# Kernel tuning notes

Hardware: AMD Instinct MI355X
Metric: run time of the kernel (lower is better)

## Reference

```python
import jax, jax.numpy as jnp
import numpy as np

B, N, E, FIN, H, D = 256, 1024, 8192, 8, 4, 5
HD = H * D            # GATv2: 4 heads * 5 dim, concat -> 20
OBS = N               # flattened obs length
AOUT = 64             # action_space_output_dim (aggregator output)
HID = 256             # hidden_size
NOUT = 64             # num_outputs (logits)
NEG = 0.2             # GATv2 leaky_relu negative slope
EPS = 1e-5            # batchnorm eps


def setup_inputs() -> dict:
    key = jax.random.key(0)
    ks = jax.random.split(key, 16)
    def lin(k, i, o):
        return (jax.random.normal(k, (i, o), jnp.float32) / np.sqrt(i)).astype(jnp.float32)
    return {
        "x": jax.random.normal(ks[0], (B, N, FIN), jnp.float32),
        "obs": jax.random.normal(ks[1], (B, OBS), jnp.float32),
        "edge_index": jax.random.randint(ks[2], (2, E), 0, N),
        # GATv2 layer 0 (in=FIN) and layer 1 (in=HD)
        "Wl0": lin(ks[3], FIN, HD), "Wr0": lin(ks[4], FIN, HD),
        "att0": (jax.random.normal(ks[5], (H, D), jnp.float32) * 0.1), "b0": jnp.zeros((HD,), jnp.float32),
        "Wl1": lin(ks[6], HD, HD), "Wr1": lin(ks[7], HD, HD),
        "att1": (jax.random.normal(ks[8], (H, D), jnp.float32) * 0.1), "b1": jnp.zeros((HD,), jnp.float32),
        # BatchNorm params per layer (over feature dim)
        "g0": jnp.ones((HD,), jnp.float32), "be0": jnp.zeros((HD,), jnp.float32),
        "g1": jnp.ones((HD,), jnp.float32), "be1": jnp.zeros((HD,), jnp.float32),
        # aggregator linear (mean pool -> action-space dim)
        "Wagg": lin(ks[9], HD, AOUT), "bagg": jnp.zeros((AOUT,), jnp.float32),
        # logits MLP: cat(agg, obs) -> HID -> HID//2 -> NOUT (tanh activations)
        "W1": lin(ks[10], AOUT + OBS, HID), "bh1": jnp.zeros((HID,), jnp.float32),
        "W2": lin(ks[11], HID, HID // 2), "bh2": jnp.zeros((HID // 2,), jnp.float32),
        "Wout": lin(ks[12], HID // 2, NOUT), "bout": jnp.zeros((NOUT,), jnp.float32),
    }


def _gatv2_single(x, src, dst, Wl, Wr, att, bias):
    # x: [N, Fin]; src/dst: [Es] (with self loops)
    xl = (x @ Wl).reshape(N, H, D)
    xr = (x @ Wr).reshape(N, H, D)
    m = jax.nn.leaky_relu(xl[src] + xr[dst], NEG)        # [Es, H, D]
    e = jnp.einsum('ehd,hd->eh', m, att)                 # [Es, H]
    emax = jax.ops.segment_max(e, dst, num_segments=N)   # every node has a self loop
    p = jnp.exp(e - emax[dst])
    s = jax.ops.segment_sum(p, dst, num_segments=N)
    alpha = p / s[dst]                                   # softmax over incoming edges
    out = jax.ops.segment_sum(alpha[:, :, None] * xl[src], dst, num_segments=N)
    return out.reshape(N, HD) + bias


def _bn(x, g, b):
    # training-mode batchnorm over all (batch, node) positions, per feature
    mu = x.mean(axis=(0, 1))
    var = x.var(axis=(0, 1))
    return (x - mu) * jax.lax.rsqrt(var + EPS) * g + b


def reference(x, obs, edge_index, Wl0, Wr0, att0, b0, Wl1, Wr1, att1, b1,
              g0, be0, g1, be1, Wagg, bagg, W1, bh1, W2, bh2, Wout, bout):
    loops = jnp.arange(N)
    src = jnp.concatenate([edge_index[0], loops])
    dst = jnp.concatenate([edge_index[1], loops])
    layer = lambda xb, Wl, Wr, att, bias: jax.vmap(
        lambda xn: _gatv2_single(xn, src, dst, Wl, Wr, att, bias))(xb)
    h = layer(x, Wl0, Wr0, att0, b0)       # [B, N, HD]
    h = _bn(h, g0, be0)
    h = layer(h, Wl1, Wr1, att1, b1)
    h = _bn(h, g1, be1)
    agg = h.mean(axis=1) @ Wagg + bagg     # mean graph pooling -> [B, AOUT]
    f = jnp.concatenate([agg, obs], axis=1)
    f = jnp.tanh(f @ W1 + bh1)
    f = jnp.tanh(f @ W2 + bh2)
    return f @ Wout + bout                 # logits [B, NOUT]
```

## Files before the change

### kernel.cpp

```cpp
#include <hip/hip_runtime.h>
#include <hip/hip_bf16.h>
#include <math.h>

typedef unsigned short u16;
typedef __attribute__((ext_vector_type(8))) short short8;
typedef __attribute__((ext_vector_type(4))) float floatx4;

constexpr int kN   = 1024;
constexpr int kB   = 256;
constexpr int kE   = 8192;
constexpr int kHD  = 20;
constexpr float kEps = 1e-5f;

static __device__ __forceinline__ float u16_bf16_to_f32(u16 v) {
  return __uint_as_float(((unsigned)v) << 16);
}
static __device__ __forceinline__ void unpack2(unsigned u, float& a, float& b) {
  a = __uint_as_float(u << 16);
  b = __uint_as_float(u & 0xffff0000u);
}
static __device__ __forceinline__ u16 f2bf(float f) {
  __hip_bfloat16 h = __float2bfloat16(f);
  return *reinterpret_cast<u16*>(&h);
}
static __device__ __forceinline__ unsigned pack_bf16(float a, float b) {
  return (unsigned)f2bf(a) | ((unsigned)f2bf(b) << 16);
}

static __device__ __forceinline__ int detect_flag(const unsigned* __restrict__ x) {
  __shared__ int sflag;
  int t = threadIdx.x;
  if (t < 64) {
    unsigned w = x[t];
    unsigned e = (w >> 7) & 0xFFu;
    unsigned long long bl = __ballot(e >= 114u && e <= 136u);
    if (t == 0) sflag = (__popcll(bl) >= 32) ? 1 : 0;
  }
  __syncthreads();
  return sflag;
}

struct SmallConv {
  const void* src[17];
  float* dst[17];
  int n[17];
};

struct PrepArgs {
  const unsigned* x;
  const int* ei;
  const void* W1; const void* W2; const void* Wout;
  SmallConv sc;
  float* x_f;
  u16* W1p; u16* W2p; u16* Woutp;
  int* csr_off; int* csr_src;
  float* sums;
};

static __device__ __forceinline__ void repack_one(const void* src, u16* dst, int c, int N, int srcbf) {
  int n = c % N;
  int t2 = c / N;
  int q = t2 & 3, kb = t2 >> 2;
  int k0 = kb * 32 + q * 8;
  u16 w[8];
  if (srcbf) {
    const u16* s = (const u16*)src;
#pragma unroll
    for (int j = 0; j < 8; j++) w[j] = s[(size_t)(k0 + j) * N + n];
  } else {
    const float* s = (const float*)src;
#pragma unroll
    for (int j = 0; j < 8; j++) w[j] = f2bf(s[(size_t)(k0 + j) * N + n]);
  }
  uint4 out;
  out.x = (unsigned)w[0] | ((unsigned)w[1] << 16);
  out.y = (unsigned)w[2] | ((unsigned)w[3] << 16);
  out.z = (unsigned)w[4] | ((unsigned)w[5] << 16);
  out.w = (unsigned)w[6] | ((unsigned)w[7] << 16);
  *((uint4*)(dst + (size_t)c * 8)) = out;
}

__global__ __launch_bounds__(256) void prep_kernel(PrepArgs pa) {
  int bid = blockIdx.x;
  int t = threadIdx.x;
  if (bid == 0) {
    __shared__ int cnt[kN];
    __shared__ int cur[kN];
    __shared__ int wsum[4];
    for (int i = t; i < kN; i += 256) cnt[i] = 0;
    __syncthreads();
    for (int e = t; e < kE; e += 256) atomicAdd(&cnt[pa.ei[kE + e]], 1);
    __syncthreads();
    int d[4], pre[4];
    int s = 0;
#pragma unroll
    for (int j = 0; j < 4; j++) { d[j] = cnt[t * 4 + j] + 1; pre[j] = s; s += d[j]; }
    int lane = t & 63;
    int v = s;
    for (int o = 1; o < 64; o <<= 1) { int u = __shfl_up(v, o); if (lane >= o) v += u; }
    if (lane == 63) wsum[t >> 6] = v;
    __syncthreads();
    int wbase = 0;
    for (int w = 0; w < (t >> 6); w++) wbase += wsum[w];
    int base = wbase + v - s;
#pragma unroll
    for (int j = 0; j < 4; j++) {
      pa.csr_off[t * 4 + j] = base + pre[j];
      cur[t * 4 + j] = base + pre[j];
    }
    if (t == 255) pa.csr_off[kN] = wbase + v;
    __syncthreads();
    for (int e = t; e < kE; e += 256) {
      int sv = pa.ei[e], dv = pa.ei[kE + e];
      int pos = atomicAdd(&cur[dv], 1);
      pa.csr_src[pos] = sv;
    }
    for (int i = t; i < kN; i += 256) {
      int pos = atomicAdd(&cur[i], 1);
      pa.csr_src[pos] = i;
    }
    return;
  }
  int flag = detect_flag(pa.x);
  if (bid == 1) {
    for (int i = t; i < 640; i += 256) pa.sums[i] = 0.f;
    for (int k = 0; k < 17; k++) {
      int n = pa.sc.n[k];
      float* d = pa.sc.dst[k];
      if (flag) {
        const u16* s = (const u16*)pa.sc.src[k];
        for (int i = t; i < n; i += 256) d[i] = u16_bf16_to_f32(s[i]);
      } else {
        const float* s = (const float*)pa.sc.src[k];
        for (int i = t; i < n; i += 256) d[i] = s[i];
      }
    }
    return;
  }
  if (bid < 158) {
    int c = (bid - 2) * 256 + t;
    if (c < 34816) repack_one(pa.W1, pa.W1p, c, 256, flag);
    else if (c < 34816 + 4096) repack_one(pa.W2, pa.W2p, c - 34816, 128, flag);
    else if (c < 34816 + 4096 + 1024) repack_one(pa.Wout, pa.Woutp, c - 34816 - 4096, 64, flag);
    return;
  }
  int rid = (bid - 158) * 256 + t;
  int b = rid >> 10, n = rid & 1023;
  float v[8];
  if (flag) {
    uint4 r = *((const uint4*)((const u16*)pa.x + (size_t)rid * 8));
    unpack2(r.x, v[0], v[1]); unpack2(r.y, v[2], v[3]);
    unpack2(r.z, v[4], v[5]); unpack2(r.w, v[6], v[7]);
  } else {
    const float4* s = (const float4*)((const float*)pa.x + (size_t)rid * 8);
    float4 r0 = s[0], r1 = s[1];
    v[0] = r0.x; v[1] = r0.y; v[2] = r0.z; v[3] = r0.w;
    v[4] = r1.x; v[5] = r1.y; v[6] = r1.z; v[7] = r1.w;
  }
  float* d = pa.x_f + ((size_t)n * kB + b) * 8;
  ((float4*)d)[0] = make_float4(v[0], v[1], v[2], v[3]);
  ((float4*)d)[1] = make_float4(v[4], v[5], v[6], v[7]);
}

__global__ __launch_bounds__(256) void lin0_kernel(const float* __restrict__ x_f,
                                                   const float* __restrict__ Wl,
                                                   u16* __restrict__ xlb) {
  __shared__ float wl[160];
  int t = threadIdx.x;
  if (t < 160) wl[t] = Wl[t];
  __syncthreads();
  int n = blockIdx.x, b = t;
  const float4* xp = (const float4*)(x_f + ((size_t)n * kB + b) * 8);
  float xi[8];
  {
    float4 v0 = xp[0], v1 = xp[1];
    xi[0] = v0.x; xi[1] = v0.y; xi[2] = v0.z; xi[3] = v0.w;
    xi[4] = v1.x; xi[5] = v1.y; xi[6] = v1.z; xi[7] = v1.w;
  }
  float ol[kHD];
#pragma unroll
  for (int f = 0; f < kHD; f++) {
    float al = 0.f;
#pragma unroll
    for (int i = 0; i < 8; i++) al = fmaf(xi[i], wl[i * kHD + f], al);
    ol[f] = al;
  }
  uint2* pl = (uint2*)(xlb + ((size_t)n * kB + b) * kHD);
#pragma unroll
  for (int k = 0; k < 5; k++)
    pl[k] = make_uint2(pack_bf16(ol[4 * k], ol[4 * k + 1]), pack_bf16(ol[4 * k + 2], ol[4 * k + 3]));
}

__global__ __launch_bounds__(256) void lin1_kernel(const u16* __restrict__ hb,
                                                   const float* __restrict__ sums0,
                                                   const float* __restrict__ g0,
                                                   const float* __restrict__ be0,
                                                   const float* __restrict__ Wl1,
                                                   u16* __restrict__ xlb) {
  __shared__ float wl[400], sbl[kHD], afold[kHD], cfold[kHD], tot[2 * kHD];
  int t = threadIdx.x;
  if (t < 2 * kHD) {
    float v = 0.f;
    for (int k = 0; k < 8; k++) v += sums0[k * 2 * kHD + t];
    tot[t] = v;
  }
  __syncthreads();
  if (t < kHD) {
    const float inv = 1.0f / (float)(kN * kB);
    float mu = tot[t] * inv;
    float var = tot[kHD + t] * inv - mu * mu;
    float a = g0[t] * rsqrtf(var + kEps);
    afold[t] = a;
    cfold[t] = be0[t] - mu * a;
  }
  __syncthreads();
  for (int idx = t; idx < 400; idx += 256) wl[idx] = afold[idx / kHD] * Wl1[idx];
  if (t < kHD) {
    float s = 0.f;
    for (int f = 0; f < kHD; f++) s += cfold[f] * Wl1[f * kHD + t];
    sbl[t] = s;
  }
  __syncthreads();
  int n = blockIdx.x, b = t;
  float hv[kHD];
  {
    const uint2* p = (const uint2*)(hb + ((size_t)n * kB + b) * kHD);
#pragma unroll
    for (int k = 0; k < 5; k++) {
      uint2 v = p[k];
      unpack2(v.x, hv[4 * k], hv[4 * k + 1]);
      unpack2(v.y, hv[4 * k + 2], hv[4 * k + 3]);
    }
  }
  float ol[kHD];
#pragma unroll
  for (int j = 0; j < kHD; j++) {
    float al = sbl[j];
#pragma unroll
    for (int f = 0; f < kHD; f++) al = fmaf(hv[f], wl[f * kHD + j], al);
    ol[j] = al;
  }
  uint2* pl = (uint2*)(xlb + ((size_t)n * kB + b) * kHD);
#pragma unroll
  for (int k = 0; k < 5; k++)
    pl[k] = make_uint2(pack_bf16(ol[4 * k], ol[4 * k + 1]), pack_bf16(ol[4 * k + 2], ol[4 * k + 3]));
}

static __device__ __forceinline__ void attn_core(const u16* __restrict__ xlb,
                                                 const int* __restrict__ csr_src,
                                                 const int* __restrict__ ssrc,
                                                 int beg, int deg, int b,
                                                 const float* satt, const float* sbias,
                                                 float (&red)[2][2 * kHD],
                                                 int n, int bsw,
                                                 u16* __restrict__ hout,
                                                 float* __restrict__ sums) {
  float xrv[kHD];
  (void)xrv;
}

__global__ __launch_bounds__(128) void attn0_kernel(const u16* __restrict__ xlb,
                                                    const float* __restrict__ x_f,
                                                    const float* __restrict__ Wr0,
                                                    const float* __restrict__ att,
                                                    const float* __restrict__ bias,
                                                    const int* __restrict__ csr_off,
                                                    const int* __restrict__ csr_src,
                                                    u16* __restrict__ hout,
                                                    float* __restrict__ sums) {
  __shared__ float satt[kHD], sbias[kHD], swr[160];
  __shared__ float red[2][2 * kHD];
  __shared__ int ssrc[128];
  int t = threadIdx.x;
  if (t < kHD) { satt[t] = att[t]; sbias[t] = bias[t]; }
  for (int i = t; i < 160; i += 128) swr[i] = Wr0[i];
  int n = blockIdx.x >> 1;
  int beg = csr_off[n], end = csr_off[n + 1];
  int deg = end - beg;
  for (int i = t; i < deg && i < 128; i += 128) ssrc[i] = csr_src[beg + i];
  __syncthreads();
  int b = ((blockIdx.x & 1) << 7) | t;
  float xrv[kHD];
  {
    const float4* xp = (const float4*)(x_f + ((size_t)n * kB + b) * 8);
    float4 v0 = xp[0], v1 = xp[1];
    float xi[8] = {v0.x, v0.y, v0.z, v0.w, v1.x, v1.y, v1.z, v1.w};
#pragma unroll
    for (int f = 0; f < kHD; f++) {
      float a = 0.f;
#pragma unroll
      for (int i = 0; i < 8; i++) a = fmaf(xi[i], swr[i * kHD + f], a);
      xrv[f] = a;
    }
  }
  float s[4] = {0.f, 0.f, 0.f, 0.f};
  float acc[kHD];
#pragma unroll
  for (int f = 0; f < kHD; f++) acc[f] = 0.f;

  auto loadrow = [&](int i, uint2 (&rr)[5]) {
    int srcn = (i < 128) ? ssrc[i] : csr_src[beg + i];
    const uint2* p = (const uint2*)(xlb + ((size_t)srcn * kB + b) * kHD);
#pragma unroll
    for (int k = 0; k < 5; k++) rr[k] = p[k];
  };
  auto consume = [&](uint2 (&rr)[5]) {
    float xs[kHD];
#pragma unroll
    for (int k = 0; k < 5; k++) {
      unpack2(rr[k].x, xs[4 * k], xs[4 * k + 1]);
      unpack2(rr[k].y, xs[4 * k + 2], xs[4 * k + 3]);
    }
#pragma unroll
    for (int hh = 0; hh < 4; hh++) {
      float e = 0.f;
#pragma unroll
      for (int d2 = 0; d2 < 5; d2++) {
        int f = hh * 5 + d2;
        float v = xs[f] + xrv[f];
        v = fmaxf(v, 0.2f * v);
        e = fmaf(v, satt[f], e);
      }
      float p = __expf(e);
      s[hh] += p;
#pragma unroll
      for (int d2 = 0; d2 < 5; d2++) {
        int f = hh * 5 + d2;
        acc[f] = fmaf(p, xs[f], acc[f]);
      }
    }
  };

  uint2 r0[5], r1[5];
  loadrow(0, r0);
  if (deg > 1) loadrow(1, r1);
  int i = 0;
  for (; i + 1 < deg; i += 2) {
    consume(r0);
    if (i + 2 < deg) loadrow(i + 2, r0);
    consume(r1);
    if (i + 3 < deg) loadrow(i + 3, r1);
  }
  if (i < deg) consume(r0);

  float hv[kHD];
#pragma unroll
  for (int hh = 0; hh < 4; hh++) {
    float inv = 1.f / s[hh];
#pragma unroll
    for (int d2 = 0; d2 < 5; d2++) {
      int f = hh * 5 + d2;
      hv[f] = fmaf(acc[f], inv, sbias[f]);
    }
  }
  {
    uint2* ph = (uint2*)(hout + ((size_t)n * kB + b) * kHD);
#pragma unroll
    for (int k = 0; k < 5; k++)
      ph[k] = make_uint2(pack_bf16(hv[4 * k], hv[4 * k + 1]), pack_bf16(hv[4 * k + 2], hv[4 * k + 3]));
  }
  int lane = t & 63, wv = t >> 6;
#pragma unroll
  for (int f = 0; f < kHD; f++) {
    float a = hv[f], q = hv[f] * hv[f];
    for (int o = 32; o > 0; o >>= 1) { a += __shfl_down(a, o); q += __shfl_down(q, o); }
    if (lane == 0) { red[wv][f] = a; red[wv][kHD + f] = q; }
  }
  __syncthreads();
  if (t < 2 * kHD) atomicAdd(&sums[(blockIdx.x & 7) * 2 * kHD + t], red[0][t] + red[1][t]);
}

__global__ __launch_bounds__(128) void attn1_kernel(const u16* __restrict__ xlb,
                                                    const u16* __restrict__ hb,
                                                    const float* __restrict__ sums0,
                                                    const float* __restrict__ g0,
                                                    const float* __restrict__ be0,
                                                    const float* __restrict__ Wr1,
                                                    const float* __restrict__ att,
                                                    const float* __restrict__ bias,
                                                    const int* __restrict__ csr_off,
                                                    const int* __restrict__ csr_src,
                                                    u16* __restrict__ hout,
                                                    float* __restrict__ sums) {
  __shared__ float satt[kHD], sbias[kHD], swr[400], sbr[kHD];
  __shared__ float afold[kHD], cfold[kHD], tot[2 * kHD];
  __shared__ float red[2][2 * kHD];
  __shared__ int ssrc[128];
  int t = threadIdx.x;
  if (t < kHD) { satt[t] = att[t]; sbias[t] = bias[t]; }
  if (t >= 64 && t < 64 + 2 * kHD) {
    int j = t - 64;
    float v = 0.f;
    for (int k = 0; k < 8; k++) v += sums0[k * 2 * kHD + j];
    tot[j] = v;
  }
  int n = blockIdx.x >> 1;
  int beg = csr_off[n], end = csr_off[n + 1];
  int deg = end - beg;
  for (int i = t; i < deg && i < 128; i += 128) ssrc[i] = csr_src[beg + i];
  __syncthreads();
  if (t < kHD) {
    const float inv = 1.0f / (float)(kN * kB);
    float mu = tot[t] * inv;
    float var = tot[kHD + t] * inv - mu * mu;
    float a = g0[t] * rsqrtf(var + kEps);
    afold[t] = a;
    cfold[t] = be0[t] - mu * a;
  }
  __syncthreads();
  for (int idx = t; idx < 400; idx += 128) swr[idx] = afold[idx / kHD] * Wr1[idx];
  if (t < kHD) {
    float sv = 0.f;
    for (int f = 0; f < kHD; f++) sv = fmaf(cfold[f], Wr1[f * kHD + t], sv);
    sbr[t] = sv;
  }
  __syncthreads();
  int b = ((blockIdx.x & 1) << 7) | t;
  float xrv[kHD];
  {
    float hv0[kHD];
    const uint2* p = (const uint2*)(hb + ((size_t)n * kB + b) * kHD);
#pragma unroll
    for (int k = 0; k < 5; k++) {
      uint2 v = p[k];
      unpack2(v.x, hv0[4 * k], hv0[4 * k + 1]);
      unpack2(v.y, hv0[4 * k + 2], hv0[4 * k + 3]);
    }
#pragma unroll
    for (int j = 0; j < kHD; j++) {
      float a = sbr[j];
#pragma unroll
      for (int f = 0; f < kHD; f++) a = fmaf(hv0[f], swr[f * kHD + j], a);
      xrv[j] = a;
    }
  }
  float s[4] = {0.f, 0.f, 0.f, 0.f};
  float acc[kHD];
#pragma unroll
  for (int f = 0; f < kHD; f++) acc[f] = 0.f;

  auto loadrow = [&](int i, uint2 (&rr)[5]) {
    int srcn = (i < 128) ? ssrc[i] : csr_src[beg + i];
    const uint2* p = (const uint2*)(xlb + ((size_t)srcn * kB + b) * kHD);
#pragma unroll
    for (int k = 0; k < 5; k++) rr[k] = p[k];
  };
  auto consume = [&](uint2 (&rr)[5]) {
    float xs[kHD];
#pragma unroll
    for (int k = 0; k < 5; k++) {
      unpack2(rr[k].x, xs[4 * k], xs[4 * k + 1]);
      unpack2(rr[k].y, xs[4 * k + 2], xs[4 * k + 3]);
    }
#pragma unroll
    for (int hh = 0; hh < 4; hh++) {
      float e = 0.f;
#pragma unroll
      for (int d2 = 0; d2 < 5; d2++) {
        int f = hh * 5 + d2;
        float v = xs[f] + xrv[f];
        v = fmaxf(v, 0.2f * v);
        e = fmaf(v, satt[f], e);
      }
      float p = __expf(e);
      s[hh] += p;
#pragma unroll
      for (int d2 = 0; d2 < 5; d2++) {
        int f = hh * 5 + d2;
        acc[f] = fmaf(p, xs[f], acc[f]);
      }
    }
  };

  uint2 r0[5], r1[5];
  loadrow(0, r0);
  if (deg > 1) loadrow(1, r1);
  int i = 0;
  for (; i + 1 < deg; i += 2) {
    consume(r0);
    if (i + 2 < deg) loadrow(i + 2, r0);
    consume(r1);
    if (i + 3 < deg) loadrow(i + 3, r1);
  }
  if (i < deg) consume(r0);

  float hv[kHD];
#pragma unroll
  for (int hh = 0; hh < 4; hh++) {
    float inv = 1.f / s[hh];
#pragma unroll
    for (int d2 = 0; d2 < 5; d2++) {
      int f = hh * 5 + d2;
      hv[f] = fmaf(acc[f], inv, sbias[f]);
    }
  }
  {
    uint2* ph = (uint2*)(hout + ((size_t)n * kB + b) * kHD);
#pragma unroll
    for (int k = 0; k < 5; k++)
      ph[k] = make_uint2(pack_bf16(hv[4 * k], hv[4 * k + 1]), pack_bf16(hv[4 * k + 2], hv[4 * k + 3]));
  }
  int lane = t & 63, wv = t >> 6;
#pragma unroll
  for (int f = 0; f < kHD; f++) {
    float a = hv[f], q = hv[f] * hv[f];
    for (int o = 32; o > 0; o >>= 1) { a += __shfl_down(a, o); q += __shfl_down(q, o); }
    if (lane == 0) { red[wv][f] = a; red[wv][kHD + f] = q; }
  }
  __syncthreads();
  if (t < 2 * kHD) atomicAdd(&sums[(blockIdx.x & 7) * 2 * kHD + t], red[0][t] + red[1][t]);
}

__global__ __launch_bounds__(256) void pool_fin_kernel(const u16* __restrict__ hb,
                                                       const float* __restrict__ sums,
                                                       const float* __restrict__ g1,
                                                       const float* __restrict__ be1,
                                                       const float* __restrict__ Wagg,
                                                       const float* __restrict__ bagg,
                                                       const void* __restrict__ obsraw,
                                                       const unsigned* __restrict__ xdet,
                                                       u16* __restrict__ finb) {
  int flag = detect_flag(xdet);
  int b = blockIdx.x, t = threadIdx.x;
  float acc[kHD];
#pragma unroll
  for (int f = 0; f < kHD; f++) acc[f] = 0.f;
  for (int n = t; n < kN; n += 256) {
    const uint2* p = (const uint2*)(hb + ((size_t)n * kB + b) * kHD);
#pragma unroll
    for (int k = 0; k < 5; k++) {
      uint2 v = p[k];
      float a0, a1, a2, a3;
      unpack2(v.x, a0, a1); unpack2(v.y, a2, a3);
      acc[4 * k] += a0; acc[4 * k + 1] += a1; acc[4 * k + 2] += a2; acc[4 * k + 3] += a3;
    }
  }
  __shared__ float red[4][kHD];
  __shared__ float tot[2 * kHD], pv[kHD];
#pragma unroll
  for (int f = 0; f < kHD; f++) {
    float v = acc[f];
    for (int o = 32; o > 0; o >>= 1) v += __shfl_down(v, o);
    if ((t & 63) == 0) red[t >> 6][f] = v;
  }
  if (t < 2 * kHD) {
    float v = 0.f;
    for (int k = 0; k < 8; k++) v += sums[k * 2 * kHD + t];
    tot[t] = v;
  }
  __syncthreads();
  if (t < kHD) {
    const float inv = 1.0f / (float)(kN * kB);
    float mu = tot[t] * inv;
    float var = tot[kHD + t] * inv - mu * mu;
    float a1 = g1[t] * rsqrtf(var + kEps);
    float c1 = be1[t] - mu * a1;
    float pool = (red[0][t] + red[1][t] + red[2][t] + red[3][t]) * (1.0f / kN);
    pv[t] = pool * a1 + c1;
  }
  __syncthreads();
  if (t < 64) {
    float agg = bagg[t];
#pragma unroll
    for (int f = 0; f < kHD; f++) agg = fmaf(pv[f], Wagg[f * 64 + t], agg);
    finb[(size_t)b * 1088 + t] = f2bf(agg);
  }
  if (t < 128) {
    uint4* dst = (uint4*)(finb + (size_t)b * 1088 + 64 + t * 8);
    if (flag) {
      *dst = *((const uint4*)((const u16*)obsraw + (size_t)b * 1024 + t * 8));
    } else {
      const float4* sp = (const float4*)((const float*)obsraw + (size_t)b * 1024 + t * 8);
      float4 r0 = sp[0], r1 = sp[1];
      uint4 o;
      o.x = pack_bf16(r0.x, r0.y); o.y = pack_bf16(r0.z, r0.w);
      o.z = pack_bf16(r1.x, r1.y); o.w = pack_bf16(r1.z, r1.w);
      *dst = o;
    }
  }
}

__global__ __launch_bounds__(256) void mlp_kernel(const u16* __restrict__ finb,
                                                  const u16* __restrict__ W1p,
                                                  const u16* __restrict__ W2p,
                                                  const u16* __restrict__ Woutp,
                                                  const float* __restrict__ bh1,
                                                  const float* __restrict__ bh2,
                                                  const float* __restrict__ bout,
                                                  const unsigned* __restrict__ xdet,
                                                  void* __restrict__ outv) {
  __shared__ __align__(16) u16 fins[16][1096];
  __shared__ __align__(16) u16 h1s[16][264];
  __shared__ __align__(16) u16 h2s[16][136];
  int flag = detect_flag(xdet);
  int t = threadIdx.x;
  int m0 = blockIdx.x * 16;
  for (int r = 0; r < 16; r++) {
    for (int k = t * 8; k < 1088; k += 2048)
      *(uint4*)&fins[r][k] = *(const uint4*)(finb + (size_t)(m0 + r) * 1088 + k);
  }
  __syncthreads();
  int wave = t >> 6, lane = t & 63, lo = lane & 15, quad = lane >> 4;
  {
    floatx4 acc[4] = {{0.f, 0.f, 0.f, 0.f}, {0.f, 0.f, 0.f, 0.f}, {0.f, 0.f, 0.f, 0.f}, {0.f, 0.f, 0.f, 0.f}};
    for (int kb = 0; kb < 34; kb++) {
      short8 a = *(const short8*)&fins[lo][kb * 32 + quad * 8];
#pragma unroll
      for (int nt = 0; nt < 4; nt++) {
        int n0 = (wave * 4 + nt) * 16;
        short8 bf = *(const short8*)(W1p + ((size_t)(kb * 4 + quad) * 256 + n0 + lo) * 8);
        acc[nt] = __builtin_amdgcn_mfma_f32_16x16x32_bf16(a, bf, acc[nt], 0, 0, 0);
      }
    }
#pragma unroll
    for (int nt = 0; nt < 4; nt++) {
      int n0 = (wave * 4 + nt) * 16;
      float bias = bh1[n0 + lo];
#pragma unroll
      for (int r = 0; r < 4; r++) h1s[quad * 4 + r][n0 + lo] = f2bf(tanhf(acc[nt][r] + bias));
    }
  }
  __syncthreads();
  {
    floatx4 acc[2] = {{0.f, 0.f, 0.f, 0.f}, {0.f, 0.f, 0.f, 0.f}};
    for (int kb = 0; kb < 8; kb++) {
      short8 a = *(const short8*)&h1s[lo][kb * 32 + quad * 8];
#pragma unroll
      for (int nt = 0; nt < 2; nt++) {
        int n0 = (wave * 2 + nt) * 16;
        short8 bf = *(const short8*)(W2p + ((size_t)(kb * 4 + quad) * 128 + n0 + lo) * 8);
        acc[nt] = __builtin_amdgcn_mfma_f32_16x16x32_bf16(a, bf, acc[nt], 0, 0, 0);
      }
    }
#pragma unroll
    for (int nt = 0; nt < 2; nt++) {
      int n0 = (wave * 2 + nt) * 16;
      float bias = bh2[n0 + lo];
#pragma unroll
      for (int r = 0; r < 4; r++) h2s[quad * 4 + r][n0 + lo] = f2bf(tanhf(acc[nt][r] + bias));
    }
  }
  __syncthreads();
  {
    int n0 = wave * 16;
    floatx4 acc = {0.f, 0.f, 0.f, 0.f};
    for (int kb = 0; kb < 4; kb++) {
      short8 a = *(const short8*)&h2s[lo][kb * 32 + quad * 8];
      short8 bf = *(const short8*)(Woutp + ((size_t)(kb * 4 + quad) * 64 + n0 + lo) * 8);
      acc = __builtin_amdgcn_mfma_f32_16x16x32_bf16(a, bf, acc, 0, 0, 0);
    }
    float bias = bout[n0 + lo];
    if (flag) {
      __hip_bfloat16* o = (__hip_bfloat16*)outv;
#pragma unroll
      for (int r = 0; r < 4; r++)
        o[(size_t)(m0 + quad * 4 + r) * 64 + n0 + lo] = __float2bfloat16(acc[r] + bias);
    } else {
      float* o = (float*)outv;
#pragma unroll
      for (int r = 0; r < 4; r++)
        o[(size_t)(m0 + quad * 4 + r) * 64 + n0 + lo] = acc[r] + bias;
    }
  }
}

extern "C" void kernel_launch(void* const* d_in, const int* in_sizes, int n_in,
                              void* d_out, int out_size, void* d_ws, size_t ws_size,
                              hipStream_t stream) {
  const int* ei = (const int*)d_in[2];
  char* ws = (char*)d_ws;

  float* sums0   = (float*)(ws + 0);
  float* sums1   = (float*)(ws + 1280);
  int*   csr_off = (int*)(ws + 2816);
  int*   csr_src = (int*)(ws + 7168);
  float* convf   = (float*)(ws + 44288);
  u16*   W1p     = (u16*)(ws + 56832);
  u16*   W2p     = (u16*)(ws + 613888);
  u16*   Woutp   = (u16*)(ws + 679424);
  u16*   finb    = (u16*)(ws + 695808);
  float* x_f     = (float*)(ws + 1253120);
  u16*   xlb     = (u16*)(ws + 9641728);
  u16*   hb      = (u16*)(ws + 20127488);
  u16*   hb2     = (u16*)(ws + 30613248);

  const int s_din[17] = {3, 4, 5, 6, 7, 8, 9, 10, 11, 12, 13, 14, 15, 16, 18, 20, 22};
  const int s_n[17]   = {160, 160, 20, 20, 400, 400, 20, 20, 20, 20, 20, 20, 1280, 64, 256, 128, 64};
  SmallConv sc;
  float* fptr[17];
  {
    size_t co = 0;
    for (int i = 0; i < 17; i++) {
      sc.src[i] = d_in[s_din[i]];
      sc.dst[i] = convf + co;
      sc.n[i] = s_n[i];
      fptr[i] = convf + co;
      co += (size_t)s_n[i];
    }
  }
  float* Wl0_f = fptr[0],  *Wr0_f = fptr[1],  *att0_f = fptr[2], *b0_f = fptr[3];
  float* Wl1_f = fptr[4],  *Wr1_f = fptr[5],  *att1_f = fptr[6], *b1_f = fptr[7];
  float* g0_f = fptr[8],   *be0_f = fptr[9],  *g1_f = fptr[10],  *be1_f = fptr[11];
  float* Wagg_f = fptr[12], *bagg_f = fptr[13], *bh1_f = fptr[14], *bh2_f = fptr[15];
  float* bout_f = fptr[16];

  PrepArgs pa;
  pa.x = (const unsigned*)d_in[0];
  pa.ei = ei;
  pa.W1 = d_in[17]; pa.W2 = d_in[19]; pa.Wout = d_in[21];
  pa.sc = sc;
  pa.x_f = x_f;
  pa.W1p = W1p; pa.W2p = W2p; pa.Woutp = Woutp;
  pa.csr_off = csr_off; pa.csr_src = csr_src;
  pa.sums = sums0;

  prep_kernel<<<1182, 256, 0, stream>>>(pa);
  lin0_kernel<<<kN, 256, 0, stream>>>(x_f, Wl0_f, xlb);
  attn0_kernel<<<2 * kN, 128, 0, stream>>>(xlb, x_f, Wr0_f, att0_f, b0_f, csr_off, csr_src, hb, sums0);
  lin1_kernel<<<kN, 256, 0, stream>>>(hb, sums0, g0_f, be0_f, Wl1_f, xlb);
  attn1_kernel<<<2 * kN, 128, 0, stream>>>(xlb, hb, sums0, g0_f, be0_f, Wr1_f, att1_f, b1_f,
                                           csr_off, csr_src, hb2, sums1);
  pool_fin_kernel<<<kB, 256, 0, stream>>>(hb2, sums1, g1_f, be1_f, Wagg_f, bagg_f,
                                          d_in[1], (const unsigned*)d_in[0], finb);
  mlp_kernel<<<16, 256, 0, stream>>>(finb, W1p, W2p, Woutp, bh1_f, bh2_f, bout_f,
                                     (const unsigned*)d_in[0], d_out);
}
```

Baseline: 239.8 us.

## Tile node features by 64-batch groups, store x as bf16, split pooling out of MLP

Node-feature buffers move to a [batch/64][node][64] tiled layout, so each 64-thread attention block gathers source rows from a compact per-tile region rather than rows strided by the full batch. The input x is kept as bf16 instead of fp32, halving that intermediate. Attention kernels go from 128 to 64 threads with twice as many blocks. Layer-1 BN statistics move from attn1 into a new pool kernel that also writes partial pooled sums, and the MLP kernel now does the BN fold, aggregator linear and obs packing itself, removing the finb buffer. The pool kernel launches only 64 blocks, which may leave much of the GPU idle.

```diff
diff --git a/kernel.cpp b/kernel.cpp
--- a/kernel.cpp
+++ b/kernel.cpp
@@ -40,6 +40,10 @@
   return sflag;
 }
 
+static __device__ __forceinline__ size_t gidx(int n, int b) {
+  return ((size_t)(b >> 6) * kN + n) * 64 + (b & 63);
+}
+
 struct SmallConv {
   const void* src[17];
   float* dst[17];
@@ -51,7 +55,7 @@
   const int* ei;
   const void* W1; const void* W2; const void* Wout;
   SmallConv sc;
-  float* x_f;
+  u16* xb;
   u16* W1p; u16* W2p; u16* Woutp;
   int* csr_off; int* csr_src;
   float* sums;
@@ -146,23 +150,19 @@
   }
   int rid = (bid - 158) * 256 + t;
   int b = rid >> 10, n = rid & 1023;
-  float v[8];
+  uint4 o;
   if (flag) {
-    uint4 r = *((const uint4*)((const u16*)pa.x + (size_t)rid * 8));
-    unpack2(r.x, v[0], v[1]); unpack2(r.y, v[2], v[3]);
-    unpack2(r.z, v[4], v[5]); unpack2(r.w, v[6], v[7]);
+    o = *((const uint4*)((const u16*)pa.x + (size_t)rid * 8));
   } else {
     const float4* s = (const float4*)((const float*)pa.x + (size_t)rid * 8);
     float4 r0 = s[0], r1 = s[1];
-    v[0] = r0.x; v[1] = r0.y; v[2] = r0.z; v[3] = r0.w;
-    v[4] = r1.x; v[5] = r1.y; v[6] = r1.z; v[7] = r1.w;
-  }
-  float* d = pa.x_f + ((size_t)n * kB + b) * 8;
-  ((float4*)d)[0] = make_float4(v[0], v[1], v[2], v[3]);
-  ((float4*)d)[1] = make_float4(v[4], v[5], v[6], v[7]);
-}
-
-__global__ __launch_bounds__(256) void lin0_kernel(const float* __restrict__ x_f,
+    o.x = pack_bf16(r0.x, r0.y); o.y = pack_bf16(r0.z, r0.w);
+    o.z = pack_bf16(r1.x, r1.y); o.w = pack_bf16(r1.z, r1.w);
+  }
+  *((uint4*)(pa.xb + ((size_t)n * kB + b) * 8)) = o;
+}
+
+__global__ __launch_bounds__(256) void lin0_kernel(const u16* __restrict__ xb,
                                                    const float* __restrict__ Wl,
                                                    u16* __restrict__ xlb) {
   __shared__ float wl[160];
@@ -170,13 +170,10 @@
   if (t < 160) wl[t] = Wl[t];
   __syncthreads();
   int n = blockIdx.x, b = t;
-  const float4* xp = (const float4*)(x_f + ((size_t)n * kB + b) * 8);
+  uint4 r = *((const uint4*)(xb + ((size_t)n * kB + b) * 8));
   float xi[8];
-  {
-    float4 v0 = xp[0], v1 = xp[1];
-    xi[0] = v0.x; xi[1] = v0.y; xi[2] = v0.z; xi[3] = v0.w;
-    xi[4] = v1.x; xi[5] = v1.y; xi[6] = v1.z; xi[7] = v1.w;
-  }
+  unpack2(r.x, xi[0], xi[1]); unpack2(r.y, xi[2], xi[3]);
+  unpack2(r.z, xi[4], xi[5]); unpack2(r.w, xi[6], xi[7]);
   float ol[kHD];
 #pragma unroll
   for (int f = 0; f < kHD; f++) {
@@ -185,7 +182,7 @@
     for (int i = 0; i < 8; i++) al = fmaf(xi[i], wl[i * kHD + f], al);
     ol[f] = al;
   }
-  uint2* pl = (uint2*)(xlb + ((size_t)n * kB + b) * kHD);
+  uint2* pl = (uint2*)(xlb + gidx(n, b) * kHD);
 #pragma unroll
   for (int k = 0; k < 5; k++)
     pl[k] = make_uint2(pack_bf16(ol[4 * k], ol[4 * k + 1]), pack_bf16(ol[4 * k + 2], ol[4 * k + 3]));
@@ -224,7 +221,7 @@
   int n = blockIdx.x, b = t;
   float hv[kHD];
   {
-    const uint2* p = (const uint2*)(hb + ((size_t)n * kB + b) * kHD);
+    const uint2* p = (const uint2*)(hb + gidx(n, b) * kHD);
 #pragma unroll
     for (int k = 0; k < 5; k++) {
       uint2 v = p[k];
@@ -240,51 +237,40 @@
     for (int f = 0; f < kHD; f++) al = fmaf(hv[f], wl[f * kHD + j], al);
     ol[j] = al;
   }
-  uint2* pl = (uint2*)(xlb + ((size_t)n * kB + b) * kHD);
+  uint2* pl = (uint2*)(xlb + gidx(n, b) * kHD);
 #pragma unroll
   for (int k = 0; k < 5; k++)
     pl[k] = make_uint2(pack_bf16(ol[4 * k], ol[4 * k + 1]), pack_bf16(ol[4 * k + 2], ol[4 * k + 3]));
 }
 
-static __device__ __forceinline__ void attn_core(const u16* __restrict__ xlb,
-                                                 const int* __restrict__ csr_src,
-                                                 const int* __restrict__ ssrc,
-                                                 int beg, int deg, int b,
-                                                 const float* satt, const float* sbias,
-                                                 float (&red)[2][2 * kHD],
-                                                 int n, int bsw,
-                                                 u16* __restrict__ hout,
-                                                 float* __restrict__ sums) {
-  float xrv[kHD];
-  (void)xrv;
-}
-
-__global__ __launch_bounds__(128) void attn0_kernel(const u16* __restrict__ xlb,
-                                                    const float* __restrict__ x_f,
-                                                    const float* __restrict__ Wr0,
-                                                    const float* __restrict__ att,
-                                                    const float* __restrict__ bias,
-                                                    const int* __restrict__ csr_off,
-                                                    const int* __restrict__ csr_src,
-                                                    u16* __restrict__ hout,
-                                                    float* __restrict__ sums) {
+__global__ __launch_bounds__(64) void attn0_kernel(const u16* __restrict__ xlb,
+                                                   const u16* __restrict__ xb,
+                                                   const float* __restrict__ Wr0,
+                                                   const float* __restrict__ att,
+                                                   const float* __restrict__ bias,
+                                                   const int* __restrict__ csr_off,
+                                                   const int* __restrict__ csr_src,
+                                                   u16* __restrict__ hout,
+                                                   float* __restrict__ sums) {
   __shared__ float satt[kHD], sbias[kHD], swr[160];
-  __shared__ float red[2][2 * kHD];
   __shared__ int ssrc[128];
+  __shared__ float red[2 * kHD];
   int t = threadIdx.x;
+  int tb = blockIdx.x & 3;
+  int n = blockIdx.x >> 2;
   if (t < kHD) { satt[t] = att[t]; sbias[t] = bias[t]; }
-  for (int i = t; i < 160; i += 128) swr[i] = Wr0[i];
-  int n = blockIdx.x >> 1;
+  for (int i = t; i < 160; i += 64) swr[i] = Wr0[i];
   int beg = csr_off[n], end = csr_off[n + 1];
   int deg = end - beg;
-  for (int i = t; i < deg && i < 128; i += 128) ssrc[i] = csr_src[beg + i];
-  __syncthreads();
-  int b = ((blockIdx.x & 1) << 7) | t;
+  for (int i = t; i < deg && i < 128; i += 64) ssrc[i] = csr_src[beg + i];
+  __syncthreads();
+  int b = (tb << 6) | t;
   float xrv[kHD];
   {
-    const float4* xp = (const float4*)(x_f + ((size_t)n * kB + b) * 8);
-    float4 v0 = xp[0], v1 = xp[1];
-    float xi[8] = {v0.x, v0.y, v0.z, v0.w, v1.x, v1.y, v1.z, v1.w};
+    uint4 r = *((const uint4*)(xb + ((size_t)n * kB + b) * 8));
+    float xi[8];
+    unpack2(r.x, xi[0], xi[1]); unpack2(r.y, xi[2], xi[3]);
+    unpack2(r.z, xi[4], xi[5]); unpack2(r.w, xi[6], xi[7]);
 #pragma unroll
     for (int f = 0; f < kHD; f++) {
       float a = 0.f;
@@ -298,9 +284,10 @@
 #pragma unroll
   for (int f = 0; f < kHD; f++) acc[f] = 0.f;
 
+  const size_t tilebase = (size_t)tb * kN * 64 * kHD;
   auto loadrow = [&](int i, uint2 (&rr)[5]) {
     int srcn = (i < 128) ? ssrc[i] : csr_src[beg + i];
-    const uint2* p = (const uint2*)(xlb + ((size_t)srcn * kB + b) * kHD);
+    const uint2* p = (const uint2*)(xlb + tilebase + ((size_t)srcn * 64 + t) * kHD);
 #pragma unroll
     for (int k = 0; k < 5; k++) rr[k] = p[k];
   };
@@ -354,50 +341,47 @@
     }
   }
   {
-    uint2* ph = (uint2*)(hout + ((size_t)n * kB + b) * kHD);
+    uint2* ph = (uint2*)(hout + tilebase + ((size_t)n * 64 + t) * kHD);
 #pragma unroll
     for (int k = 0; k < 5; k++)
       ph[k] = make_uint2(pack_bf16(hv[4 * k], hv[4 * k + 1]), pack_bf16(hv[4 * k + 2], hv[4 * k + 3]));
   }
-  int lane = t & 63, wv = t >> 6;
 #pragma unroll
   for (int f = 0; f < kHD; f++) {
     float a = hv[f], q = hv[f] * hv[f];
     for (int o = 32; o > 0; o >>= 1) { a += __shfl_down(a, o); q += __shfl_down(q, o); }
-    if (lane == 0) { red[wv][f] = a; red[wv][kHD + f] = q; }
-  }
-  __syncthreads();
-  if (t < 2 * kHD) atomicAdd(&sums[(blockIdx.x & 7) * 2 * kHD + t], red[0][t] + red[1][t]);
-}
-
-__global__ __launch_bounds__(128) void attn1_kernel(const u16* __restrict__ xlb,
-                                                    const u16* __restrict__ hb,
-                                                    const float* __restrict__ sums0,
-                                                    const float* __restrict__ g0,
-                                                    const float* __restrict__ be0,
-                                                    const float* __restrict__ Wr1,
-                                                    const float* __restrict__ att,
-                                                    const float* __restrict__ bias,
-                                                    const int* __restrict__ csr_off,
-                                                    const int* __restrict__ csr_src,
-                                                    u16* __restrict__ hout,
-                                                    float* __restrict__ sums) {
+    if (t == 0) { red[f] = a; red[kHD + f] = q; }
+  }
+  __syncthreads();
+  if (t < 2 * kHD) atomicAdd(&sums[(blockIdx.x & 7) * 2 * kHD + t], red[t]);
+}
+
+__global__ __launch_bounds__(64) void attn1_kernel(const u16* __restrict__ xlb,
+                                                   const u16* __restrict__ hb,
+                                                   const float* __restrict__ sums0,
+                                                   const float* __restrict__ g0,
+                                                   const float* __restrict__ be0,
+                                                   const float* __restrict__ Wr1,
+                                                   const float* __restrict__ att,
+                                                   const float* __restrict__ bias,
+                                                   const int* __restrict__ csr_off,
+                                                   const int* __restrict__ csr_src,
+                                                   u16* __restrict__ hout) {
   __shared__ float satt[kHD], sbias[kHD], swr[400], sbr[kHD];
   __shared__ float afold[kHD], cfold[kHD], tot[2 * kHD];
-  __shared__ float red[2][2 * kHD];
   __shared__ int ssrc[128];
   int t = threadIdx.x;
+  int tb = blockIdx.x & 3;
+  int n = blockIdx.x >> 2;
   if (t < kHD) { satt[t] = att[t]; sbias[t] = bias[t]; }
-  if (t >= 64 && t < 64 + 2 * kHD) {
-    int j = t - 64;
+  if (t < 2 * kHD) {
     float v = 0.f;
-    for (int k = 0; k < 8; k++) v += sums0[k * 2 * kHD + j];
-    tot[j] = v;
-  }
-  int n = blockIdx.x >> 1;
+    for (int k = 0; k < 8; k++) v += sums0[k * 2 * kHD + t];
+    tot[t] = v;
+  }
   int beg = csr_off[n], end = csr_off[n + 1];
   int deg = end - beg;
-  for (int i = t; i < deg && i < 128; i += 128) ssrc[i] = csr_src[beg + i];
+  for (int i = t; i < deg && i < 128; i += 64) ssrc[i] = csr_src[beg + i];
   __syncthreads();
   if (t < kHD) {
     const float inv = 1.0f / (float)(kN * kB);
@@ -408,18 +392,18 @@
     cfold[t] = be0[t] - mu * a;
   }
   __syncthreads();
-  for (int idx = t; idx < 400; idx += 128) swr[idx] = afold[idx / kHD] * Wr1[idx];
+  for (int idx = t; idx < 400; idx += 64) swr[idx] = afold[idx / kHD] * Wr1[idx];
   if (t < kHD) {
     float sv = 0.f;
     for (int f = 0; f < kHD; f++) sv = fmaf(cfold[f], Wr1[f * kHD + t], sv);
     sbr[t] = sv;
   }
   __syncthreads();
-  int b = ((blockIdx.x & 1) << 7) | t;
+  const size_t tilebase = (size_t)tb * kN * 64 * kHD;
   float xrv[kHD];
   {
     float hv0[kHD];
-    const uint2* p = (const uint2*)(hb + ((size_t)n * kB + b) * kHD);
+    const uint2* p = (const uint2*)(hb + tilebase + ((size_t)n * 64 + t) * kHD);
 #pragma unroll
     for (int k = 0; k < 5; k++) {
       uint2 v = p[k];
@@ -441,7 +425,7 @@
 
   auto loadrow = [&](int i, uint2 (&rr)[5]) {
     int srcn = (i < 128) ? ssrc[i] : csr_src[beg + i];
-    const uint2* p = (const uint2*)(xlb + ((size_t)srcn * kB + b) * kHD);
+    const uint2* p = (const uint2*)(xlb + tilebase + ((size_t)srcn * 64 + t) * kHD);
 #pragma unroll
     for (int k = 0; k < 5; k++) rr[k] = p[k];
   };
@@ -494,93 +478,59 @@
       hv[f] = fmaf(acc[f], inv, sbias[f]);
     }
   }
-  {
-    uint2* ph = (uint2*)(hout + ((size_t)n * kB + b) * kHD);
-#pragma unroll
-    for (int k = 0; k < 5; k++)
-      ph[k] = make_uint2(pack_bf16(hv[4 * k], hv[4 * k + 1]), pack_bf16(hv[4 * k + 2], hv[4 * k + 3]));
-  }
-  int lane = t & 63, wv = t >> 6;
-#pragma unroll
-  for (int f = 0; f < kHD; f++) {
-    float a = hv[f], q = hv[f] * hv[f];
-    for (int o = 32; o > 0; o >>= 1) { a += __shfl_down(a, o); q += __shfl_down(q, o); }
-    if (lane == 0) { red[wv][f] = a; red[wv][kHD + f] = q; }
-  }
-  __syncthreads();
-  if (t < 2 * kHD) atomicAdd(&sums[(blockIdx.x & 7) * 2 * kHD + t], red[0][t] + red[1][t]);
-}
-
-__global__ __launch_bounds__(256) void pool_fin_kernel(const u16* __restrict__ hb,
-                                                       const float* __restrict__ sums,
-                                                       const float* __restrict__ g1,
-                                                       const float* __restrict__ be1,
-                                                       const float* __restrict__ Wagg,
-                                                       const float* __restrict__ bagg,
-                                                       const void* __restrict__ obsraw,
-                                                       const unsigned* __restrict__ xdet,
-                                                       u16* __restrict__ finb) {
-  int flag = detect_flag(xdet);
-  int b = blockIdx.x, t = threadIdx.x;
-  float acc[kHD];
-#pragma unroll
-  for (int f = 0; f < kHD; f++) acc[f] = 0.f;
-  for (int n = t; n < kN; n += 256) {
-    const uint2* p = (const uint2*)(hb + ((size_t)n * kB + b) * kHD);
+  uint2* ph = (uint2*)(hout + tilebase + ((size_t)n * 64 + t) * kHD);
+#pragma unroll
+  for (int k = 0; k < 5; k++)
+    ph[k] = make_uint2(pack_bf16(hv[4 * k], hv[4 * k + 1]), pack_bf16(hv[4 * k + 2], hv[4 * k + 3]));
+}
+
+__global__ __launch_bounds__(64) void pool_kernel(const u16* __restrict__ hb2,
+                                                  float* __restrict__ pool_part,
+                                                  float* __restrict__ sums1) {
+  __shared__ float red[2 * kHD];
+  int t = threadIdx.x;
+  int tb = blockIdx.x & 3;
+  int ch = blockIdx.x >> 2;
+  const size_t tilebase = (size_t)tb * kN * 64 * kHD;
+  float acc[kHD], q[kHD];
+#pragma unroll
+  for (int f = 0; f < kHD; f++) { acc[f] = 0.f; q[f] = 0.f; }
+  for (int j = 0; j < 64; j++) {
+    int n = ch * 64 + j;
+    const uint2* p = (const uint2*)(hb2 + tilebase + ((size_t)n * 64 + t) * kHD);
 #pragma unroll
     for (int k = 0; k < 5; k++) {
       uint2 v = p[k];
       float a0, a1, a2, a3;
       unpack2(v.x, a0, a1); unpack2(v.y, a2, a3);
-      acc[4 * k] += a0; acc[4 * k + 1] += a1; acc[4 * k + 2] += a2; acc[4 * k + 3] += a3;
-    }
-  }
-  __shared__ float red[4][kHD];
-  __shared__ float tot[2 * kHD], pv[kHD];
+      acc[4 * k] += a0;     q[4 * k] += a0 * a0;
+      acc[4 * k + 1] += a1; q[4 * k + 1] += a1 * a1;
+      acc[4 * k + 2] += a2; q[4 * k + 2] += a2 * a2;
+      acc[4 * k + 3] += a3; q[4 * k + 3] += a3 * a3;
+    }
+  }
+  int b = tb * 64 + t;
+  float4* pp = (float4*)(pool_part + ((size_t)ch * kB + b) * kHD);
+#pragma unroll
+  for (int k = 0; k < 5; k++)
+    pp[k] = make_float4(acc[4 * k], acc[4 * k + 1], acc[4 * k + 2], acc[4 * k + 3]);
 #pragma unroll
   for (int f = 0; f < kHD; f++) {
-    float v = acc[f];
-    for (int o = 32; o > 0; o >>= 1) v += __shfl_down(v, o);
-    if ((t & 63) == 0) red[t >> 6][f] = v;
-  }
-  if (t < 2 * kHD) {
-    float v = 0.f;
-    for (int k = 0; k < 8; k++) v += sums[k * 2 * kHD + t];
-    tot[t] = v;
-  }
-  __syncthreads();
-  if (t < kHD) {
-    const float inv = 1.0f / (float)(kN * kB);
-    float mu = tot[t] * inv;
-    float var = tot[kHD + t] * inv - mu * mu;
-    float a1 = g1[t] * rsqrtf(var + kEps);
-    float c1 = be1[t] - mu * a1;
-    float pool = (red[0][t] + red[1][t] + red[2][t] + red[3][t]) * (1.0f / kN);
-    pv[t] = pool * a1 + c1;
-  }
-  __syncthreads();
-  if (t < 64) {
-    float agg = bagg[t];
-#pragma unroll
-    for (int f = 0; f < kHD; f++) agg = fmaf(pv[f], Wagg[f * 64 + t], agg);
-    finb[(size_t)b * 1088 + t] = f2bf(agg);
-  }
-  if (t < 128) {
-    uint4* dst = (uint4*)(finb + (size_t)b * 1088 + 64 + t * 8);
-    if (flag) {
-      *dst = *((const uint4*)((const u16*)obsraw + (size_t)b * 1024 + t * 8));
-    } else {
-      const float4* sp = (const float4*)((const float*)obsraw + (size_t)b * 1024 + t * 8);
-      float4 r0 = sp[0], r1 = sp[1];
-      uint4 o;
-      o.x = pack_bf16(r0.x, r0.y); o.y = pack_bf16(r0.z, r0.w);
-      o.z = pack_bf16(r1.x, r1.y); o.w = pack_bf16(r1.z, r1.w);
-      *dst = o;
-    }
-  }
-}
-
-__global__ __launch_bounds__(256) void mlp_kernel(const u16* __restrict__ finb,
+    float a = acc[f], qq = q[f];
+    for (int o = 32; o > 0; o >>= 1) { a += __shfl_down(a, o); qq += __shfl_down(qq, o); }
+    if (t == 0) { red[f] = a; red[kHD + f] = qq; }
+  }
+  __syncthreads();
+  if (t < 2 * kHD) atomicAdd(&sums1[(blockIdx.x & 7) * 2 * kHD + t], red[t]);
+}
+
+__global__ __launch_bounds__(256) void mlp_kernel(const float* __restrict__ pool_part,
+                                                  const float* __restrict__ sums1,
+                                                  const float* __restrict__ g1,
+                                                  const float* __restrict__ be1,
+                                                  const float* __restrict__ Wagg,
+                                                  const float* __restrict__ bagg,
+                                                  const void* __restrict__ obsraw,
                                                   const u16* __restrict__ W1p,
                                                   const u16* __restrict__ W2p,
                                                   const u16* __restrict__ Woutp,
@@ -592,12 +542,54 @@
   __shared__ __align__(16) u16 fins[16][1096];
   __shared__ __align__(16) u16 h1s[16][264];
   __shared__ __align__(16) u16 h2s[16][136];
+  __shared__ float sWagg[1280], pv[16][kHD], a1[kHD], c1[kHD], tot[2 * kHD];
   int flag = detect_flag(xdet);
   int t = threadIdx.x;
   int m0 = blockIdx.x * 16;
-  for (int r = 0; r < 16; r++) {
-    for (int k = t * 8; k < 1088; k += 2048)
-      *(uint4*)&fins[r][k] = *(const uint4*)(finb + (size_t)(m0 + r) * 1088 + k);
+  if (t < 2 * kHD) {
+    float v = 0.f;
+    for (int k = 0; k < 8; k++) v += sums1[k * 2 * kHD + t];
+    tot[t] = v;
+  }
+  for (int idx = t; idx < 1280; idx += 256) sWagg[idx] = Wagg[idx];
+  __syncthreads();
+  if (t < kHD) {
+    const float inv = 1.0f / (float)(kN * kB);
+    float mu = tot[t] * inv;
+    float var = tot[kHD + t] * inv - mu * mu;
+    float a = g1[t] * rsqrtf(var + kEps);
+    a1[t] = a;
+    c1[t] = be1[t] - mu * a;
+  }
+  __syncthreads();
+  for (int idx = t; idx < 16 * kHD; idx += 256) {
+    int bl = idx / kHD, f = idx % kHD;
+    float p = 0.f;
+    for (int ch = 0; ch < 16; ch++) p += pool_part[((size_t)ch * kB + m0 + bl) * kHD + f];
+    pv[bl][f] = (p * (1.0f / kN)) * a1[f] + c1[f];
+  }
+  for (int idx = t * 8; idx < 16 * 1024; idx += 2048) {
+    int r = idx >> 10, c = idx & 1023;
+    uint4 o;
+    if (flag) {
+      o = *((const uint4*)((const u16*)obsraw + (size_t)(m0 + r) * 1024 + c));
+    } else {
+      const float4* sp = (const float4*)((const float*)obsraw + (size_t)(m0 + r) * 1024 + c);
+      float4 r0 = sp[0], r1 = sp[1];
+      o.x = pack_bf16(r0.x, r0.y); o.y = pack_bf16(r0.z, r0.w);
+      o.z = pack_bf16(r1.x, r1.y); o.w = pack_bf16(r1.z, r1.w);
+    }
+    *(uint4*)&fins[r][64 + c] = o;
+  }
+  __syncthreads();
+  {
+    int j = t & 63, rg = t >> 6;
+    for (int r = rg; r < 16; r += 4) {
+      float a = bagg[j];
+#pragma unroll
+      for (int f = 0; f < kHD; f++) a = fmaf(pv[r][f], sWagg[f * 64 + j], a);
+      fins[r][j] = f2bf(a);
+    }
   }
   __syncthreads();
   int wave = t >> 6, lane = t & 63, lo = lane & 15, quad = lane >> 4;
@@ -670,19 +662,19 @@
   const int* ei = (const int*)d_in[2];
   char* ws = (char*)d_ws;
 
-  float* sums0   = (float*)(ws + 0);
-  float* sums1   = (float*)(ws + 1280);
-  int*   csr_off = (int*)(ws + 2816);
-  int*   csr_src = (int*)(ws + 7168);
-  float* convf   = (float*)(ws + 44288);
-  u16*   W1p     = (u16*)(ws + 56832);
-  u16*   W2p     = (u16*)(ws + 613888);
-  u16*   Woutp   = (u16*)(ws + 679424);
-  u16*   finb    = (u16*)(ws + 695808);
-  float* x_f     = (float*)(ws + 1253120);
-  u16*   xlb     = (u16*)(ws + 9641728);
-  u16*   hb      = (u16*)(ws + 20127488);
-  u16*   hb2     = (u16*)(ws + 30613248);
+  float* sums0     = (float*)(ws + 0);
+  float* sums1     = (float*)(ws + 1280);
+  int*   csr_off   = (int*)(ws + 2816);
+  int*   csr_src   = (int*)(ws + 7168);
+  float* convf     = (float*)(ws + 44288);
+  u16*   W1p       = (u16*)(ws + 56832);
+  u16*   W2p       = (u16*)(ws + 613888);
+  u16*   Woutp     = (u16*)(ws + 679424);
+  float* pool_part = (float*)(ws + 695808);
+  u16*   xb        = (u16*)(ws + 1023744);
+  u16*   xlb       = (u16*)(ws + 5218048);
+  u16*   hb        = (u16*)(ws + 15703808);
+  u16*   hb2       = (u16*)(ws + 26189568);
 
   const int s_din[17] = {3, 4, 5, 6, 7, 8, 9, 10, 11, 12, 13, 14, 15, 16, 18, 20, 22};
   const int s_n[17]   = {160, 160, 20, 20, 400, 400, 20, 20, 20, 20, 20, 20, 1280, 64, 256, 128, 64};
@@ -709,19 +701,19 @@
   pa.ei = ei;
   pa.W1 = d_in[17]; pa.W2 = d_in[19]; pa.Wout = d_in[21];
   pa.sc = sc;
-  pa.x_f = x_f;
+  pa.xb = xb;
   pa.W1p = W1p; pa.W2p = W2p; pa.Woutp = Woutp;
   pa.csr_off = csr_off; pa.csr_src = csr_src;
   pa.sums = sums0;
 
   prep_kernel<<<1182, 256, 0, stream>>>(pa);
-  lin0_kernel<<<kN, 256, 0, stream>>>(x_f, Wl0_f, xlb);
-  attn0_kernel<<<2 * kN, 128, 0, stream>>>(xlb, x_f, Wr0_f, att0_f, b0_f, csr_off, csr_src, hb, sums0);
+  lin0_kernel<<<kN, 256, 0, stream>>>(xb, Wl0_f, xlb);
+  attn0_kernel<<<4 * kN, 64, 0, stream>>>(xlb, xb, Wr0_f, att0_f, b0_f, csr_off, csr_src, hb, sums0);
   lin1_kernel<<<kN, 256, 0, stream>>>(hb, sums0, g0_f, be0_f, Wl1_f, xlb);
-  attn1_kernel<<<2 * kN, 128, 0, stream>>>(xlb, hb, sums0, g0_f, be0_f, Wr1_f, att1_f, b1_f,
-                                           csr_off, csr_src, hb2, sums1);
-  pool_fin_kernel<<<kB, 256, 0, stream>>>(hb2, sums1, g1_f, be1_f, Wagg_f, bagg_f,
-                                          d_in[1], (const unsigned*)d_in[0], finb);
-  mlp_kernel<<<16, 256, 0, stream>>>(finb, W1p, W2p, Woutp, bh1_f, bh2_f, bout_f,
+  attn1_kernel<<<4 * kN, 64, 0, stream>>>(xlb, hb, sums0, g0_f, be0_f, Wr1_f, att1_f, b1_f,
+                                          csr_off, csr_src, hb2);
+  pool_kernel<<<64, 64, 0, stream>>>(hb2, pool_part, sums1);
+  mlp_kernel<<<16, 256, 0, stream>>>(pool_part, sums1, g1_f, be1_f, Wagg_f, bagg_f, d_in[1],
+                                     W1p, W2p, Woutp, bh1_f, bh2_f, bout_f,
                                      (const unsigned*)d_in[0], d_out);
 }
```

Measured after the change: 260.5 us. +8.6%, slower.
